# Kernel tuning notes

Hardware: AMD Instinct MI355X
Metric: run time of the kernel (lower is better)

## Reference

```python
import jax, jax.numpy as jnp
import numpy as np

D_KEY, BANK_N = 128, 9720
BS, N = 1, 1620          # n = h*w = 30*54 (480p features, stride 16)
D_VAL, C, OBJ_N = 512, 512, 3


def setup_inputs() -> dict:
    key = jax.random.key(0)
    k1, k2, k3, k4, k5 = jax.random.split(key, 5)
    return {
        "keys_bank": jax.random.normal(k1, (D_KEY, BANK_N), dtype=jnp.float32),
        "q_in": jax.random.normal(k2, (BS, D_KEY, N), dtype=jnp.float32),
        "q_out": jax.random.normal(k3, (OBJ_N, C, N), dtype=jnp.float32),
        "values": jax.random.normal(k4, (OBJ_N, D_VAL, BANK_N), dtype=jnp.float32),
        "masks": jax.random.uniform(k5, (OBJ_N, 1, BANK_N), dtype=jnp.float32),
    }


def reference(keys_bank, q_in, q_out, values, masks):
    # p[b,k,n] = softmax_k( keys^T q_in / sqrt(d_key) )
    d_key = keys_bank.shape[0]
    scale = 1.0 / np.sqrt(d_key).astype(np.float32)
    p = jnp.einsum("dk,bdn->bkn", keys_bank, q_in) * scale
    p = jax.nn.softmax(p, axis=1)  # over bank dim

    # Batched over objects (original loops per object, sharing p)
    mem = jnp.einsum("ovk,bkn->obvn", values, p)       # (obj, bs, d_val, n)
    mask_mem = jnp.einsum("ouk,bkn->obun", masks, p)   # (obj, bs, 1, n)
    q_out_with_mask = q_out[:, None, :, :] * mask_mem  # (obj, bs, C, n)

    out = jnp.concatenate([mem, q_out_with_mask], axis=2)  # (obj, bs, d_val+C, n)
    return jnp.swapaxes(out, 0, 1)                          # (bs, obj, d_val+C, n)
```

## Files before the change

### kernel.cpp

```cpp
#include <hip/hip_runtime.h>
#include <hip/hip_bf16.h>

typedef unsigned short u16;
typedef unsigned char  u8;

#define D_KEY   128
#define BANK_N  9720
#define BANK_P  9728
#define N_TOK   1620
#define N_PAD   1664
#define OBJ_N   3
#define M_PAD   1664
#define LDCOL   1664
#define ONES_ROW 1539
#define QK_SCALE 0.08838834764831845f

typedef __bf16 bf16x8 __attribute__((ext_vector_type(8)));
typedef float  f32x4  __attribute__((ext_vector_type(4)));
typedef unsigned int u32x4 __attribute__((ext_vector_type(4)));

__device__ __forceinline__ float bf2f(u16 u) {
  union { unsigned int i; float f; } v; v.i = ((unsigned int)u) << 16; return v.f;
}
__device__ __forceinline__ u16 f2bf(float f) {
  unsigned int x = __float_as_uint(f);
  unsigned int r = x + 0x7fffu + ((x >> 16) & 1u);
  return (u16)(r >> 16);
}
__device__ __forceinline__ unsigned pack_fp8x4(float a, float b, float c, float d) {
  unsigned v = __builtin_amdgcn_cvt_pk_fp8_f32(a, b, 0, false);
  v = __builtin_amdgcn_cvt_pk_fp8_f32(c, d, v, true);
  return v;
}
__device__ __forceinline__ u8 f2fp8(float a) {
  return (u8)(__builtin_amdgcn_cvt_pk_fp8_f32(a, 0.f, 0, false) & 0xff);
}

__device__ __forceinline__ void load_lds16(const void* g, void* l) {
  __builtin_amdgcn_global_load_lds(
      (const __attribute__((address_space(1))) void*)g,
      (__attribute__((address_space(3))) void*)l, 16, 0, 0);
}

__global__ void prep(const float* __restrict__ q, const float* __restrict__ keys,
                     const float* __restrict__ values, const float* __restrict__ masks,
                     u16* __restrict__ qT, u16* __restrict__ kT, u8* __restrict__ vm8) {
  __shared__ float t[64][65];
  int b = blockIdx.x;
  if (b < 832) {
    int idx = b * 256 + threadIdx.x;
    int n = idx >> 7, d = idx & 127;
    float v = (n < N_TOK) ? q[d * N_TOK + n] * QK_SCALE : 0.f;
    qT[idx] = f2bf(v);
    return;
  }
  if (b < 1136) {
    b -= 832;
    const int bk = (b % 152) * 64;
    const int bd = (b / 152) * 64;
    const int tx = threadIdx.x & 63;
    const int ty = threadIdx.x >> 6;
#pragma unroll
    for (int i = 0; i < 64; i += 4) {
      int d = bd + ty + i;
      int k = bk + tx;
      t[ty + i][tx] = (k < BANK_N) ? keys[(size_t)d * BANK_N + k] : 0.f;
    }
    __syncthreads();
#pragma unroll
    for (int i = 0; i < 64; i += 4) {
      int r = ty + i;
      kT[(size_t)(bk + r) * D_KEY + bd + tx] = f2bf(t[tx][r]);
    }
    return;
  }
  const int NV = BANK_P / 4;
  int idx = (b - 1136) * 256 + threadIdx.x;
  if (idx >= M_PAD * NV) return;
  int m = idx / NV;
  int k4 = (idx - m * NV) * 4;
  float4 v = make_float4(0.f, 0.f, 0.f, 0.f);
  if (m == ONES_ROW) {
    v.x = (k4     < BANK_N) ? 1.f : 0.f;
    v.y = (k4 + 1 < BANK_N) ? 1.f : 0.f;
    v.z = (k4 + 2 < BANK_N) ? 1.f : 0.f;
    v.w = (k4 + 3 < BANK_N) ? 1.f : 0.f;
  } else {
    const float* src = nullptr;
    if (m < 1536)          src = values + (size_t)m * BANK_N;
    else if (m < ONES_ROW) src = masks + (size_t)(m - 1536) * BANK_N;
    if (src) {
      if (k4 + 3 < BANK_N) v = *(const float4*)(src + k4);
      else {
        if (k4     < BANK_N) v.x = src[k4];
        if (k4 + 1 < BANK_N) v.y = src[k4 + 1];
        if (k4 + 2 < BANK_N) v.z = src[k4 + 2];
        if (k4 + 3 < BANK_N) v.w = src[k4 + 3];
      }
    }
  }
  *(unsigned*)(vm8 + (size_t)m * BANK_P + k4) = pack_fp8x4(v.x, v.y, v.z, v.w);
}

__global__ void gemm_qk(const u16* __restrict__ A, const u16* __restrict__ B,
                        u8* __restrict__ E8)
{
  __shared__ __align__(16) u16 sbuf[8192];
  u16* As = sbuf;
  u16* Bs = sbuf + 4096;

  const int tid  = threadIdx.x;
  const int wave = tid >> 6;
  const int lane = tid & 63;
  const int bn = blockIdx.x % 76, bm = blockIdx.x / 76;

  const u16* Abase = A + (size_t)bm * 128 * D_KEY;
  const u16* Bbase = B + (size_t)bn * 128 * D_KEY;

  const int r  = lane >> 2;
  const int c8 = (lane & 3) << 3;
  const int s0 = wave, s1 = wave + 4;

  f32x4 acc[4][4];
#pragma unroll
  for (int i = 0; i < 4; i++)
#pragma unroll
    for (int j = 0; j < 4; j++) acc[i][j] = (f32x4){0.f, 0.f, 0.f, 0.f};

  const int m_in = lane & 15;
  const int quad = lane >> 4;
  const int wm = (wave >> 1) * 64;
  const int wn = (wave & 1) * 64;

  for (int kt = 0; kt < D_KEY; kt += 32) {
    load_lds16(Abase + (size_t)(s0 * 16 + r) * D_KEY + kt + c8, &As[s0 * 512]);
    load_lds16(Abase + (size_t)(s1 * 16 + r) * D_KEY + kt + c8, &As[s1 * 512]);
    load_lds16(Bbase + (size_t)(s0 * 16 + r) * D_KEY + kt + c8, &Bs[s0 * 512]);
    load_lds16(Bbase + (size_t)(s1 * 16 + r) * D_KEY + kt + c8, &Bs[s1 * 512]);
    __syncthreads();

    bf16x8 af[4], bfr[4];
#pragma unroll
    for (int i = 0; i < 4; i++)
      af[i] = *(const bf16x8*)&As[(wm + i * 16 + m_in) * 32 + quad * 8];
#pragma unroll
    for (int j = 0; j < 4; j++)
      bfr[j] = *(const bf16x8*)&Bs[(wn + j * 16 + m_in) * 32 + quad * 8];
#pragma unroll
    for (int i = 0; i < 4; i++)
#pragma unroll
      for (int j = 0; j < 4; j++)
        acc[i][j] = __builtin_amdgcn_mfma_f32_16x16x32_bf16(af[i], bfr[j], acc[i][j], 0, 0, 0);
    __syncthreads();
  }

  u8* sb8 = (u8*)sbuf;
#pragma unroll
  for (int i = 0; i < 4; i++)
#pragma unroll
    for (int j = 0; j < 4; j++)
#pragma unroll
      for (int t = 0; t < 4; t++) {
        int row_l = wm + i * 16 + quad * 4 + t;
        int col_l = wn + j * 16 + m_in;
        bool valid = (bn * 128 + col_l) < BANK_N;
        sb8[(row_l << 7) + col_l] = valid ? f2fp8(__expf(acc[i][j][t])) : (u8)0;
      }
  __syncthreads();

  for (int chunk = tid; chunk < 1024; chunk += 256) {
    int row = chunk >> 3;
    int cu  = (chunk & 7) << 4;
    u32x4 v = *(const u32x4*)&sb8[(row << 7) + cu];
    *(u32x4*)&E8[(size_t)(bm * 128 + row) * BANK_P + bn * 128 + cu] = v;
  }
}

__global__ __launch_bounds__(256, 4)
void gemm_pv(const u8* __restrict__ A, const u8* __restrict__ B,
             u16* __restrict__ memC, int kChunk, size_t cPartStride)
{
  __shared__ __align__(16) u16 sbuf[8192];
  u8* As8 = (u8*)sbuf;
  u8* Bs8 = (u8*)sbuf + 4096;

  const int tid  = threadIdx.x;
  const int wave = tid >> 6;
  const int lane = tid & 63;

  int b = blockIdx.x;
  int bz = b / 169;
  int rr = b - bz * 169;
  int gid = rr / 52;
  int rem = rr - gid * 52;
  int width = (gid < 3) ? 4 : 1;
  int bm = rem / width;
  int bn = gid * 4 + (rem - bm * width);

  const int kbeg = bz * kChunk;
  const int kend = kbeg + kChunk;

  const u8* Abase = A + (size_t)bm * 128 * BANK_P;
  const u8* Bbase = B + (size_t)bn * 128 * BANK_P;

  const int srow  = lane >> 1;
  const int shalf = (((lane & 1) ^ ((lane >> 3) & 1)) << 4);

  f32x4 acc[4][4];
#pragma unroll
  for (int i = 0; i < 4; i++)
#pragma unroll
    for (int j = 0; j < 4; j++) acc[i][j] = (f32x4){0.f, 0.f, 0.f, 0.f};

  const int m_in = lane & 15;
  const int quad = lane >> 4;
  const int wm = (wave >> 1) * 64;
  const int wn = (wave & 1) * 64;
  const int fxor = ((m_in >> 2) & 1) << 4;

  for (int kt = kbeg; kt < kend; kt += 32) {
    load_lds16(Abase + (size_t)(wave * 32 + srow) * BANK_P + kt + shalf, As8 + wave * 1024);
    load_lds16(Bbase + (size_t)(wave * 32 + srow) * BANK_P + kt + shalf, Bs8 + wave * 1024);
    __syncthreads();

    long af[4], bfr[4];
#pragma unroll
    for (int i = 0; i < 4; i++)
      af[i] = *(const long*)&As8[(wm + i * 16 + m_in) * 32 + (quad * 8 ^ fxor)];
#pragma unroll
    for (int j = 0; j < 4; j++)
      bfr[j] = *(const long*)&Bs8[(wn + j * 16 + m_in) * 32 + (quad * 8 ^ fxor)];
#pragma unroll
    for (int i = 0; i < 4; i++)
#pragma unroll
      for (int j = 0; j < 4; j++)
        acc[i][j] = __builtin_amdgcn_mfma_f32_16x16x32_fp8_fp8(af[i], bfr[j], acc[i][j], 0, 0, 0);
    __syncthreads();
  }

  u16* Cg = memC + (size_t)bz * cPartStride;
#pragma unroll
  for (int h = 0; h < 2; h++) {
    __syncthreads();
    if ((wave >> 1) == h) {
#pragma unroll
      for (int i = 0; i < 4; i++)
#pragma unroll
        for (int j = 0; j < 4; j++)
#pragma unroll
          for (int t = 0; t < 4; t++) {
            int row_l = i * 16 + quad * 4 + t;
            int col_l = wn + j * 16 + m_in;
            sbuf[(row_l << 7) + col_l] = f2bf(acc[i][j][t]);
          }
    }
    __syncthreads();
    for (int chunk = tid; chunk < 1024; chunk += 256) {
      int row = chunk >> 4;
      int cu  = (chunk & 15) << 3;
      u32x4 v = *(const u32x4*)&sbuf[(row << 7) + cu];
      __builtin_nontemporal_store(
          v, (u32x4*)&Cg[(size_t)(bm * 128 + h * 64 + row) * LDCOL + bn * 128 + cu]);
    }
  }
}

__global__ void epilogue(const u16* __restrict__ memC, const float* __restrict__ q_out,
                         float* __restrict__ out, int nParts) {
  const int NV = N_TOK / 4;
  int idx = blockIdx.x * 256 + threadIdx.x;
  if (idx >= OBJ_N * 1024 * NV) return;
  int n4 = (idx % NV) * 4;
  int t = idx / NV;
  int c = t & 1023;
  int o = t >> 10;
  const size_t ps = (size_t)M_PAD * LDCOL;

  const u16* lbase = memC + (size_t)ONES_ROW * LDCOL + n4;
  float4 l = make_float4(0.f, 0.f, 0.f, 0.f);
  for (int z = 0; z < nParts; z++) {
    ushort4 v = *(const ushort4*)(lbase + z * ps);
    l.x += bf2f(v.x); l.y += bf2f(v.y); l.z += bf2f(v.z); l.w += bf2f(v.w);
  }

  size_t rowoff = (c < 512) ? (size_t)(o * 512 + c) * LDCOL
                            : (size_t)(1536 + o) * LDCOL;
  const u16* base = memC + rowoff + n4;
  float4 s = make_float4(0.f, 0.f, 0.f, 0.f);
  for (int z = 0; z < nParts; z++) {
    ushort4 v = *(const ushort4*)(base + z * ps);
    s.x += bf2f(v.x); s.y += bf2f(v.y); s.z += bf2f(v.z); s.w += bf2f(v.w);
  }
  float4 rv;
  float ix = 1.f / l.x, iy = 1.f / l.y, iz = 1.f / l.z, iw = 1.f / l.w;
  if (c < 512) {
    rv.x = s.x * ix; rv.y = s.y * iy; rv.z = s.z * iz; rv.w = s.w * iw;
  } else {
    float4 q = *(const float4*)(q_out + (size_t)(o * 512 + (c - 512)) * N_TOK + n4);
    rv.x = q.x * s.x * ix; rv.y = q.y * s.y * iy;
    rv.z = q.z * s.z * iz; rv.w = q.w * s.w * iw;
  }
  *(float4*)(out + (size_t)(o * 1024 + c) * N_TOK + n4) = rv;
}

extern "C" void kernel_launch(void* const* d_in, const int* in_sizes, int n_in,
                              void* d_out, int out_size, void* d_ws, size_t ws_size,
                              hipStream_t stream) {
  const float* keys   = (const float*)d_in[0];
  const float* q_in   = (const float*)d_in[1];
  const float* q_out  = (const float*)d_in[2];
  const float* values = (const float*)d_in[3];
  const float* masks  = (const float*)d_in[4];
  float* out = (float*)d_out;

  char* ws = (char*)d_ws;
  size_t off = 0;
  auto alloc = [&](size_t bytes) -> void* {
    void* p = ws + off; off += (bytes + 255) & ~(size_t)255; return p;
  };
  u16* qT  = (u16*)alloc((size_t)N_PAD * D_KEY * 2);
  u16* kT  = (u16*)alloc((size_t)BANK_P * D_KEY * 2);
  u8*  vm8 = (u8*)alloc((size_t)M_PAD * BANK_P);
  u8*  E8  = (u8*)alloc((size_t)N_PAD * BANK_P);

  int nParts = 4;
  while (nParts > 1 && off + (size_t)nParts * M_PAD * LDCOL * 2 > ws_size) nParts >>= 1;
  u16* memC = (u16*)alloc((size_t)nParts * M_PAD * LDCOL * 2);

  const int vmBlocks = (M_PAD * (BANK_P / 4) + 255) / 256;
  prep<<<1136 + vmBlocks, 256, 0, stream>>>(q_in, keys, values, masks, qT, kT, vm8);

  gemm_qk<<<988, 256, 0, stream>>>(qT, kT, E8);

  int kChunk = BANK_P / nParts;
  gemm_pv<<<dim3(169 * nParts), 256, 0, stream>>>(vm8, E8, memC, kChunk, (size_t)M_PAD * LDCOL);

  epilogue<<<(OBJ_N * 1024 * (N_TOK / 4) + 255) / 256, 256, 0, stream>>>(
      memC, q_out, out, nParts);
}
```

Measured before the change: 207.4 us.

## Use 16x16x128 scaled FP8 MFMA with 128-wide K tiles in PV GEMM

The PV GEMM now stages four 32-wide K slices per iteration (128 K per barrier pair) into doubled LDS buffers. Each lane's 32-byte fragment is then fed to the gfx950 mfma_scale_f32_16x16x128_f8f6f4 instruction with unit scales, replacing four 16x16x32 fp8 MFMAs. This cuts barrier count and MFMA issue overhead and uses the wider FP8 MFMA. In exchange LDS use per block doubles and launch bounds drop occupancy to 3 blocks. The K reduction order is also changed: each lane's data now comes from one 32-wide slice, which relies on kChunk being a multiple of 128.

```diff
diff --git a/kernel.cpp b/kernel.cpp
--- a/kernel.cpp
+++ b/kernel.cpp
@@ -18,6 +18,7 @@
 typedef __bf16 bf16x8 __attribute__((ext_vector_type(8)));
 typedef float  f32x4  __attribute__((ext_vector_type(4)));
 typedef unsigned int u32x4 __attribute__((ext_vector_type(4)));
+typedef int i32x8 __attribute__((ext_vector_type(8)));
 
 __device__ __forceinline__ float bf2f(u16 u) {
   union { unsigned int i; float f; } v; v.i = ((unsigned int)u) << 16; return v.f;
@@ -176,13 +177,13 @@
   }
 }
 
-__global__ __launch_bounds__(256, 4)
+__global__ __launch_bounds__(256, 3)
 void gemm_pv(const u8* __restrict__ A, const u8* __restrict__ B,
              u16* __restrict__ memC, int kChunk, size_t cPartStride)
 {
-  __shared__ __align__(16) u16 sbuf[8192];
+  __shared__ __align__(16) u16 sbuf[16384];
   u8* As8 = (u8*)sbuf;
-  u8* Bs8 = (u8*)sbuf + 4096;
+  u8* Bs8 = (u8*)sbuf + 16384;
 
   const int tid  = threadIdx.x;
   const int wave = tid >> 6;
@@ -218,23 +219,39 @@
   const int wn = (wave & 1) * 64;
   const int fxor = ((m_in >> 2) & 1) << 4;
 
-  for (int kt = kbeg; kt < kend; kt += 32) {
-    load_lds16(Abase + (size_t)(wave * 32 + srow) * BANK_P + kt + shalf, As8 + wave * 1024);
-    load_lds16(Bbase + (size_t)(wave * 32 + srow) * BANK_P + kt + shalf, Bs8 + wave * 1024);
-    __syncthreads();
-
-    long af[4], bfr[4];
-#pragma unroll
-    for (int i = 0; i < 4; i++)
-      af[i] = *(const long*)&As8[(wm + i * 16 + m_in) * 32 + (quad * 8 ^ fxor)];
-#pragma unroll
-    for (int j = 0; j < 4; j++)
-      bfr[j] = *(const long*)&Bs8[(wn + j * 16 + m_in) * 32 + (quad * 8 ^ fxor)];
-#pragma unroll
-    for (int i = 0; i < 4; i++)
-#pragma unroll
-      for (int j = 0; j < 4; j++)
-        acc[i][j] = __builtin_amdgcn_mfma_f32_16x16x32_fp8_fp8(af[i], bfr[j], acc[i][j], 0, 0, 0);
+  const size_t arow_off = (size_t)(wave * 32 + srow) * BANK_P;
+
+  for (int kt = kbeg; kt < kend; kt += 128) {
+#pragma unroll
+    for (int s = 0; s < 4; s++)
+      load_lds16(Abase + arow_off + kt + s * 32 + shalf, As8 + s * 4096 + wave * 1024);
+#pragma unroll
+    for (int s = 0; s < 4; s++)
+      load_lds16(Bbase + arow_off + kt + s * 32 + shalf, Bs8 + s * 4096 + wave * 1024);
+    __syncthreads();
+
+    i32x8 a8[4];
+#pragma unroll
+    for (int i = 0; i < 4; i++) {
+      const u8* p = As8 + quad * 4096 + (wm + i * 16 + m_in) * 32;
+      u32x4 lo = *(const u32x4*)(p + fxor);
+      u32x4 hi = *(const u32x4*)(p + (fxor ^ 16));
+      a8[i] = (i32x8){(int)lo[0], (int)lo[1], (int)lo[2], (int)lo[3],
+                      (int)hi[0], (int)hi[1], (int)hi[2], (int)hi[3]};
+    }
+#pragma unroll
+    for (int j = 0; j < 4; j++) {
+      const u8* p = Bs8 + quad * 4096 + (wn + j * 16 + m_in) * 32;
+      u32x4 lo = *(const u32x4*)(p + fxor);
+      u32x4 hi = *(const u32x4*)(p + (fxor ^ 16));
+      i32x8 b8 = (i32x8){(int)lo[0], (int)lo[1], (int)lo[2], (int)lo[3],
+                         (int)hi[0], (int)hi[1], (int)hi[2], (int)hi[3]};
+#pragma unroll
+      for (int i = 0; i < 4; i++)
+        acc[i][j] = __builtin_amdgcn_mfma_scale_f32_16x16x128_f8f6f4(
+            a8[i], b8, acc[i][j], 0, 0,
+            0, 0x7f7f7f7f, 0, 0x7f7f7f7f);
+    }
     __syncthreads();
   }
 
```

New measurement: 192.2 us. -7.3%, faster.
